# Kernel optimization log

Hardware: AMD Instinct MI355X
Metric: run time of the kernel (lower is better)

Reference implementation:

```python
import jax, jax.numpy as jnp
import numpy as np

N_HEAD = 16
D = 1024
LV = 2048
HEAD_DIM = D // N_HEAD
B = 2
LQ = 2048
LN_EPS = 1e-5


def setup_inputs() -> dict:
    key = jax.random.key(0)
    ks = jax.random.split(key, 8)
    s = 0.02
    v = jax.random.normal(ks[0], (B, LV, D), dtype=jnp.float32)
    q = jax.random.normal(ks[1], (B, LQ, D), dtype=jnp.float32)
    # per-head attn linear: d -> lv
    Wa = jax.random.normal(ks[2], (N_HEAD, D, LV), dtype=jnp.float32) * s
    ba = jnp.zeros((N_HEAD, LV), dtype=jnp.float32)
    # per-head layernorm over d
    gamma = jnp.ones((N_HEAD, D), dtype=jnp.float32)
    beta = jnp.zeros((N_HEAD, D), dtype=jnp.float32)
    # per-head proj (FilteredLinear modeled as affine): d -> head_dim
    Wp = jax.random.normal(ks[3], (N_HEAD, D, HEAD_DIM), dtype=jnp.float32) * s
    bp = jnp.zeros((N_HEAD, HEAD_DIM), dtype=jnp.float32)
    return {"v": v, "q": q, "Wa": Wa, "ba": ba, "gamma": gamma,
            "beta": beta, "Wp": Wp, "bp": bp}


def _mha(v, q, Wa, ba, gamma, beta, Wp, bp):
    # attn: [H, B, Lq, Lv] = relu(q @ Wa_h + ba_h)  (batched across heads)
    attn = jax.nn.relu(jnp.einsum('bqd,hdl->hbql', q, Wa)
                       + ba[:, None, None, :])
    # external-attention aggregation: [H, B, Lq, D]
    agg = jnp.einsum('hbql,bld->hbqd', attn, v)
    # per-head LayerNorm over last dim (d)
    mu = jnp.mean(agg, axis=-1, keepdims=True)
    var = jnp.var(agg, axis=-1, keepdims=True)
    normed = (agg - mu) * jax.lax.rsqrt(var + LN_EPS)
    normed = normed * gamma[:, None, None, :] + beta[:, None, None, :]
    # per-head projection to head_dim: [H, B, Lq, head_dim]
    heads = jnp.einsum('hbqd,hde->hbqe', normed, Wp) + bp[:, None, None, :]
    # concat heads along feature dim -> [B, Lq, D]
    return heads.transpose(1, 2, 0, 3).reshape(q.shape[0], q.shape[1], -1)


def reference(v, q, Wa, ba, gamma, beta, Wp, bp):
    return _mha(v, q, Wa, ba, gamma, beta, Wp, bp)
```

## Files before the change

kernel.cpp:

```cpp
#include <hip/hip_runtime.h>
#include <hip/hip_bf16.h>

typedef __attribute__((ext_vector_type(8))) short short8;
typedef __attribute__((ext_vector_type(4))) float f32x4;

#define N_HEAD 16
#define DMODEL 1024
#define LV 2048
#define LQ 2048
#define BATCH 2
#define HEAD_DIM 64

template <int N> struct IC { static constexpr int v = N; };

__device__ inline ushort f2bf(float f) {
    union { float f; unsigned u; } v; v.f = f;
    unsigned r = v.u + 0x7fffu + ((v.u >> 16) & 1u);
    return (ushort)(r >> 16);
}
__device__ inline float bf2f(ushort h) {
    union { unsigned u; float f; } v; v.u = ((unsigned)h) << 16;
    return v.f;
}

__global__ __launch_bounds__(256) void cast_bf16(const float* __restrict__ src,
                                                 ushort* __restrict__ dst, int n) {
    int i = (blockIdx.x * 256 + threadIdx.x) * 4;
    if (i < n) {
        float4 v = *(const float4*)(src + i);
        ushort4 o;
        o.x = f2bf(v.x); o.y = f2bf(v.y); o.z = f2bf(v.z); o.w = f2bf(v.w);
        *(ushort4*)(dst + i) = o;
    }
}

__global__ __launch_bounds__(256) void transpose_cast(const float* __restrict__ src,
                                                      ushort* __restrict__ dst,
                                                      int R, int C) {
    __shared__ float t[32][33];
    size_t zoff = (size_t)blockIdx.z * R * C;
    int c0 = blockIdx.x * 32, r0 = blockIdx.y * 32;
    int tx = threadIdx.x, ty = threadIdx.y;
#pragma unroll
    for (int i = 0; i < 4; ++i)
        t[ty + i * 8][tx] = src[zoff + (size_t)(r0 + ty + i * 8) * C + c0 + tx];
    __syncthreads();
#pragma unroll
    for (int i = 0; i < 4; ++i)
        dst[zoff + (size_t)(c0 + ty + i * 8) * R + r0 + tx] = f2bf(t[tx][ty + i * 8]);
}

template <bool RELU>
__global__ __launch_bounds__(512, 4) void gemm128x256(
    const ushort* __restrict__ A, const ushort* __restrict__ B,
    ushort* __restrict__ Cout, const float* __restrict__ bias,
    int K,
    long sA_b, long sA_h, long sB_b, long sB_h, long sC_z, int ldc, long sBias_h)
{
    __shared__ __align__(16) char smem[3 * 24576];

    const int z = blockIdx.z, b = z & 1, h = z >> 1;
    A += (size_t)b * sA_b + (size_t)h * sA_h;
    B += (size_t)b * sB_b + (size_t)h * sB_h;
    const float* biasp = bias ? bias + (size_t)h * sBias_h : nullptr;

    const int bm0 = blockIdx.y * 128;
    const int bn0 = blockIdx.x * 256;
    const int T = threadIdx.x;
    const int lane = T & 63, wid = T >> 6;
    const int wr = wid >> 2, wc = wid & 3;
    const int fr = lane & 15, fq = lane >> 4;
    const int laneoff = fr * 64 + ((fq * 16) ^ ((fr >> 3) << 5));

    const int s_row = T >> 2;
    const int s_csw = ((T & 3) * 16) ^ (((T >> 5) & 1) << 5);
    const ushort* gA = A + (size_t)(bm0 + s_row) * K + (s_csw >> 1);
    const ushort* gB = B + (size_t)(bn0 + s_row) * K + (s_csw >> 1);

    const int nt = K >> 5;

    auto stage = [&](int sb, int kt) {
        char* base = smem + sb * 24576;
        const ushort* srcA = gA + (size_t)kt * 32;
        __builtin_amdgcn_global_load_lds(
            (const __attribute__((address_space(1))) void*)srcA,
            (__attribute__((address_space(3))) void*)(base + (T << 4)), 16, 0, 0);
#pragma unroll
        for (int j = 0; j < 2; ++j) {
            const ushort* srcB = gB + (size_t)j * 128 * K + (size_t)kt * 32;
            __builtin_amdgcn_global_load_lds(
                (const __attribute__((address_space(1))) void*)srcB,
                (__attribute__((address_space(3))) void*)(base + 8192 + j * 8192 + (T << 4)),
                16, 0, 0);
        }
    };

    f32x4 acc[4][4];
#pragma unroll
    for (int m = 0; m < 4; ++m)
#pragma unroll
        for (int n = 0; n < 4; ++n)
#pragma unroll
            for (int j = 0; j < 4; ++j) acc[m][n][j] = 0.f;

    auto step = [&](int t, int rb, int sb, auto DOST, auto VM) {
        const char* base = smem + rb * 24576;
        const char* pA = base + wr * 4096 + laneoff;
        const char* pB = base + 8192 + wc * 4096 + laneoff;
        short8 a[4], bb[4];
#pragma unroll
        for (int m = 0; m < 4; ++m) a[m] = *(const short8*)(pA + m * 1024);
#pragma unroll
        for (int n = 0; n < 4; ++n) bb[n] = *(const short8*)(pB + n * 1024);
        if constexpr (decltype(DOST)::v) stage(sb, t + 2);
        asm volatile("s_waitcnt lgkmcnt(0)" ::: "memory");
        __builtin_amdgcn_sched_barrier(0);
        __builtin_amdgcn_s_setprio(1);
#pragma unroll
        for (int m = 0; m < 4; ++m)
#pragma unroll
            for (int n = 0; n < 4; ++n)
                acc[m][n] = __builtin_amdgcn_mfma_f32_16x16x32_bf16(
                    a[m], bb[n], acc[m][n], 0, 0, 0);
        __builtin_amdgcn_s_setprio(0);
        __builtin_amdgcn_sched_barrier(0);
        constexpr int vm = decltype(VM)::v;
        if constexpr (vm == 3) asm volatile("s_waitcnt vmcnt(3)" ::: "memory");
        else if constexpr (vm == 0) asm volatile("s_waitcnt vmcnt(0)" ::: "memory");
        if constexpr (vm >= 0) asm volatile("s_barrier" ::: "memory");
    };

    stage(0, 0); stage(1, 1);
    asm volatile("s_waitcnt vmcnt(3)" ::: "memory");
    asm volatile("s_barrier" ::: "memory");

    int rb = 0, sb = 2;
    for (int t = 0; t < nt - 2; ++t) {
        step(t, rb, sb, IC<1>{}, IC<3>{});
        rb = (rb == 2) ? 0 : rb + 1;
        sb = (sb == 2) ? 0 : sb + 1;
    }
    step(nt - 2, rb, sb, IC<0>{}, IC<0>{});
    rb = (rb == 2) ? 0 : rb + 1;
    step(nt - 1, rb, sb, IC<0>{}, IC<-1>{});

    ushort* C = Cout + (size_t)z * sC_z;
    const int row0 = bm0 + wr * 64;
    const int col0 = bn0 + wc * 64;
#pragma unroll
    for (int n = 0; n < 4; ++n) {
        const int c = col0 + n * 16 + fr;
        const float bvv = biasp ? biasp[c] : 0.f;
#pragma unroll
        for (int m = 0; m < 4; ++m) {
            const int r = row0 + m * 16 + fq * 4;
#pragma unroll
            for (int j = 0; j < 4; ++j) {
                float val = acc[m][n][j] + bvv;
                if (RELU) val = fmaxf(val, 0.f);
                C[(size_t)(r + j) * ldc + c] = f2bf(val);
            }
        }
    }
}

__global__ __launch_bounds__(256) void ln_kernel(ushort* __restrict__ agg,
                                                 const float* __restrict__ gamma,
                                                 const float* __restrict__ beta) {
    const int wid = threadIdx.x >> 6, lane = threadIdx.x & 63;
    const size_t row = (size_t)blockIdx.x * 4 + wid;
    const int h = (int)(row >> 12);
    ushort* p = agg + row * 1024 + lane * 16;
    short8 r0 = *(const short8*)p;
    short8 r1 = *(const short8*)(p + 8);
    float x[16];
#pragma unroll
    for (int j = 0; j < 8; ++j) { x[j] = bf2f((ushort)r0[j]); x[8 + j] = bf2f((ushort)r1[j]); }
    float s = 0.f, s2 = 0.f;
#pragma unroll
    for (int j = 0; j < 16; ++j) { s += x[j]; s2 += x[j] * x[j]; }
    for (int o = 1; o < 64; o <<= 1) {
        s  += __shfl_xor(s,  o, 64);
        s2 += __shfl_xor(s2, o, 64);
    }
    float mu  = s * (1.0f / 1024.0f);
    float var = s2 * (1.0f / 1024.0f) - mu * mu;
    float rs  = rsqrtf(fmaxf(var, 0.f) + 1e-5f);
    const float* g  = gamma + (size_t)h * 1024 + lane * 16;
    const float* bt = beta  + (size_t)h * 1024 + lane * 16;
    short8 o0, o1;
#pragma unroll
    for (int j = 0; j < 8; ++j) {
        o0[j] = (short)f2bf((x[j]     - mu) * rs * g[j]     + bt[j]);
        o1[j] = (short)f2bf((x[8 + j] - mu) * rs * g[8 + j] + bt[8 + j]);
    }
    *(short8*)p = o0;
    *(short8*)(p + 8) = o1;
}

__global__ __launch_bounds__(256) void proj_kernel(const ushort* __restrict__ normed,
                                                   const ushort* __restrict__ WpT,
                                                   const float* __restrict__ bp,
                                                   float* __restrict__ out,
                                                   int h_base) {
    const int z = blockIdx.y, b = z & 1, h = z >> 1;
    const int hg = h_base + h;
    const int wid = threadIdx.x >> 6, lane = threadIdx.x & 63;
    const int fr = lane & 15, fq = lane >> 4;
    const int m0 = (blockIdx.x * 4 + wid) * 16;

    const ushort* Abase = normed + ((size_t)z * 2048 + m0 + fr) * 1024 + fq * 8;
    const ushort* Bbase = WpT + (size_t)hg * 64 * 1024 + (size_t)fr * 1024 + fq * 8;

    f32x4 acc[4];
#pragma unroll
    for (int n = 0; n < 4; ++n)
#pragma unroll
        for (int j = 0; j < 4; ++j) acc[n][j] = 0.f;

    for (int kt = 0; kt < 32; ++kt) {
        short8 a = *(const short8*)(Abase + kt * 32);
#pragma unroll
        for (int n = 0; n < 4; ++n) {
            short8 bb = *(const short8*)(Bbase + n * 16 * 1024 + kt * 32);
            acc[n] = __builtin_amdgcn_mfma_f32_16x16x32_bf16(a, bb, acc[n], 0, 0, 0);
        }
    }
#pragma unroll
    for (int n = 0; n < 4; ++n) {
        int c = hg * 64 + n * 16 + fr;
        float bvv = bp[hg * 64 + n * 16 + fr];
#pragma unroll
        for (int j = 0; j < 4; ++j)
            out[(size_t)b * 2048 * 1024 + (size_t)(m0 + fq * 4 + j) * 1024 + c] =
                acc[n][j] + bvv;
    }
}

extern "C" void kernel_launch(void* const* d_in, const int* in_sizes, int n_in,
                              void* d_out, int out_size, void* d_ws, size_t ws_size,
                              hipStream_t stream) {
    const float* v     = (const float*)d_in[0];
    const float* q     = (const float*)d_in[1];
    const float* Wa    = (const float*)d_in[2];
    const float* ba    = (const float*)d_in[3];
    const float* gamma = (const float*)d_in[4];
    const float* beta  = (const float*)d_in[5];
    const float* Wp    = (const float*)d_in[6];
    const float* bp    = (const float*)d_in[7];
    float* out = (float*)d_out;

    const size_t MB = 1ull << 20;
    char* ws = (char*)d_ws;
    ushort* qbf = (ushort*)(ws);
    ushort* vT  = (ushort*)(ws + 8 * MB);
    ushort* WpT = (ushort*)(ws + 16 * MB);
    int NH = 1;
    {
        const int cands[5] = {16, 8, 4, 2, 1};
        for (int i = 0; i < 5; ++i) {
            if ((size_t)(18 + 28 * cands[i]) * MB <= ws_size) { NH = cands[i]; break; }
        }
    }
    ushort* WaT_c  = (ushort*)(ws + 18 * MB);
    ushort* attn_c = (ushort*)(ws + (18 + (size_t)4 * NH) * MB);
    ushort* agg_c  = (ushort*)(ws + (18 + (size_t)20 * NH) * MB);

    dim3 tb(32, 8);
    cast_bf16<<<4096, 256, 0, stream>>>(q, qbf, BATCH * LQ * DMODEL);
    transpose_cast<<<dim3(DMODEL / 32, LV / 32, BATCH), tb, 0, stream>>>(v, vT, LV, DMODEL);
    transpose_cast<<<dim3(HEAD_DIM / 32, DMODEL / 32, N_HEAD), tb, 0, stream>>>(Wp, WpT, DMODEL, HEAD_DIM);

    for (int h0 = 0; h0 < N_HEAD; h0 += NH) {
        transpose_cast<<<dim3(LV / 32, DMODEL / 32, NH), tb, 0, stream>>>(
            Wa + (size_t)h0 * DMODEL * LV, WaT_c, DMODEL, LV);

        gemm128x256<true><<<dim3(LV / 256, LQ / 128, NH * 2), 512, 0, stream>>>(
            qbf, WaT_c, attn_c, ba + (size_t)h0 * LV, DMODEL,
            (long)LQ * DMODEL, 0L,
            0L, (long)LV * DMODEL,
            (long)LQ * LV, LV, (long)LV);

        gemm128x256<false><<<dim3(DMODEL / 256, LQ / 128, NH * 2), 512, 0, stream>>>(
            attn_c, vT, agg_c, nullptr, LV,
            (long)LQ * LV, (long)2 * LQ * LV,
            (long)DMODEL * LV, 0L,
            (long)LQ * DMODEL, DMODEL, 0L);

        ln_kernel<<<(NH * 2 * LQ) / 4, 256, 0, stream>>>(
            agg_c, gamma + (size_t)h0 * DMODEL, beta + (size_t)h0 * DMODEL);

        proj_kernel<<<dim3(LQ / 64, NH * 2), 256, 0, stream>>>(
            agg_c, WpT, bp, out, h0);
    }
}
```

Before: 845.3 us.

## Fuse LayerNorm into projection, stage GEMM epilogue via LDS, remap block order for XCDs

```diff
diff --git a/kernel.cpp b/kernel.cpp
--- a/kernel.cpp
+++ b/kernel.cpp
@@ -50,7 +50,7 @@
         dst[zoff + (size_t)(c0 + ty + i * 8) * R + r0 + tx] = f2bf(t[tx][ty + i * 8]);
 }
 
-template <bool RELU>
+template <bool RELU, int LNBN, int ZSH>
 __global__ __launch_bounds__(512, 4) void gemm128x256(
     const ushort* __restrict__ A, const ushort* __restrict__ B,
     ushort* __restrict__ Cout, const float* __restrict__ bias,
@@ -59,13 +59,19 @@
 {
     __shared__ __align__(16) char smem[3 * 24576];
 
-    const int z = blockIdx.z, b = z & 1, h = z >> 1;
+    const int gid = blockIdx.x;
+    const int per = (int)gridDim.x >> 3;
+    const int w = (gid & 7) * per + (gid >> 3);
+    const int z = w >> ZSH;
+    const int rem = w & ((1 << ZSH) - 1);
+    const int bm0 = (rem >> LNBN) * 128;
+    const int bn0 = (rem & ((1 << LNBN) - 1)) * 256;
+
+    const int b = z & 1, h = z >> 1;
     A += (size_t)b * sA_b + (size_t)h * sA_h;
     B += (size_t)b * sB_b + (size_t)h * sB_h;
     const float* biasp = bias ? bias + (size_t)h * sBias_h : nullptr;
 
-    const int bm0 = blockIdx.y * 128;
-    const int bn0 = blockIdx.x * 256;
     const int T = threadIdx.x;
     const int lane = T & 63, wid = T >> 6;
     const int wr = wid >> 2, wc = wid & 3;
@@ -144,73 +150,63 @@
     rb = (rb == 2) ? 0 : rb + 1;
     step(nt - 1, rb, sb, IC<0>{}, IC<-1>{});
 
-    ushort* C = Cout + (size_t)z * sC_z;
+    asm volatile("s_waitcnt vmcnt(0) lgkmcnt(0)" ::: "memory");
+    __builtin_amdgcn_s_barrier();
+    char* eb = smem + wid * 9216;
     const int row0 = bm0 + wr * 64;
     const int col0 = bn0 + wc * 64;
 #pragma unroll
     for (int n = 0; n < 4; ++n) {
-        const int c = col0 + n * 16 + fr;
-        const float bvv = biasp ? biasp[c] : 0.f;
+        const float bvv = biasp ? biasp[col0 + n * 16 + fr] : 0.f;
 #pragma unroll
         for (int m = 0; m < 4; ++m) {
-            const int r = row0 + m * 16 + fq * 4;
 #pragma unroll
             for (int j = 0; j < 4; ++j) {
                 float val = acc[m][n][j] + bvv;
                 if (RELU) val = fmaxf(val, 0.f);
-                C[(size_t)(r + j) * ldc + c] = f2bf(val);
+                *(ushort*)(eb + (m * 16 + fq * 4 + j) * 144 + (n * 16 + fr) * 2) = f2bf(val);
             }
         }
     }
-}
-
-__global__ __launch_bounds__(256) void ln_kernel(ushort* __restrict__ agg,
-                                                 const float* __restrict__ gamma,
-                                                 const float* __restrict__ beta) {
-    const int wid = threadIdx.x >> 6, lane = threadIdx.x & 63;
-    const size_t row = (size_t)blockIdx.x * 4 + wid;
-    const int h = (int)(row >> 12);
-    ushort* p = agg + row * 1024 + lane * 16;
-    short8 r0 = *(const short8*)p;
-    short8 r1 = *(const short8*)(p + 8);
-    float x[16];
-#pragma unroll
-    for (int j = 0; j < 8; ++j) { x[j] = bf2f((ushort)r0[j]); x[8 + j] = bf2f((ushort)r1[j]); }
-    float s = 0.f, s2 = 0.f;
-#pragma unroll
-    for (int j = 0; j < 16; ++j) { s += x[j]; s2 += x[j] * x[j]; }
-    for (int o = 1; o < 64; o <<= 1) {
-        s  += __shfl_xor(s,  o, 64);
-        s2 += __shfl_xor(s2, o, 64);
-    }
-    float mu  = s * (1.0f / 1024.0f);
-    float var = s2 * (1.0f / 1024.0f) - mu * mu;
-    float rs  = rsqrtf(fmaxf(var, 0.f) + 1e-5f);
-    const float* g  = gamma + (size_t)h * 1024 + lane * 16;
-    const float* bt = beta  + (size_t)h * 1024 + lane * 16;
-    short8 o0, o1;
-#pragma unroll
-    for (int j = 0; j < 8; ++j) {
-        o0[j] = (short)f2bf((x[j]     - mu) * rs * g[j]     + bt[j]);
-        o1[j] = (short)f2bf((x[8 + j] - mu) * rs * g[8 + j] + bt[8 + j]);
-    }
-    *(short8*)p = o0;
-    *(short8*)(p + 8) = o1;
-}
-
-__global__ __launch_bounds__(256) void proj_kernel(const ushort* __restrict__ normed,
-                                                   const ushort* __restrict__ WpT,
-                                                   const float* __restrict__ bp,
-                                                   float* __restrict__ out,
-                                                   int h_base) {
-    const int z = blockIdx.y, b = z & 1, h = z >> 1;
-    const int hg = h_base + h;
+    asm volatile("s_waitcnt lgkmcnt(0)" ::: "memory");
+    ushort* C = Cout + (size_t)z * sC_z;
+    const int rl = lane >> 3, cb = lane & 7;
+#pragma unroll
+    for (int i = 0; i < 8; ++i) {
+        short8 vv = *(const short8*)(eb + (i * 8 + rl) * 144 + cb * 16);
+        *(short8*)(C + (size_t)(row0 + i * 8 + rl) * ldc + col0 + cb * 8) = vv;
+    }
+}
+
+__global__ __launch_bounds__(256) void lnproj_kernel(const ushort* __restrict__ agg,
+                                                     const ushort* __restrict__ WpT,
+                                                     const float* __restrict__ gamma,
+                                                     const float* __restrict__ beta,
+                                                     const float* __restrict__ bp,
+                                                     float* __restrict__ out,
+                                                     int h_base) {
+    const int z = blockIdx.y, b = z & 1, hg = h_base + (z >> 1);
     const int wid = threadIdx.x >> 6, lane = threadIdx.x & 63;
     const int fr = lane & 15, fq = lane >> 4;
     const int m0 = (blockIdx.x * 4 + wid) * 16;
 
-    const ushort* Abase = normed + ((size_t)z * 2048 + m0 + fr) * 1024 + fq * 8;
+    const ushort* Arow = agg + ((size_t)z * 2048 + m0 + fr) * 1024 + fq * 8;
+
+    float s = 0.f, s2 = 0.f;
+    for (int kt = 0; kt < 32; ++kt) {
+        short8 a = *(const short8*)(Arow + kt * 32);
+#pragma unroll
+        for (int j = 0; j < 8; ++j) { float x = bf2f((ushort)a[j]); s += x; s2 += x * x; }
+    }
+    s  += __shfl_xor(s, 16, 64);  s2 += __shfl_xor(s2, 16, 64);
+    s  += __shfl_xor(s, 32, 64);  s2 += __shfl_xor(s2, 32, 64);
+    const float mu  = s * (1.0f / 1024.0f);
+    const float var = s2 * (1.0f / 1024.0f) - mu * mu;
+    const float rs  = rsqrtf(fmaxf(var, 0.f) + 1e-5f);
+
     const ushort* Bbase = WpT + (size_t)hg * 64 * 1024 + (size_t)fr * 1024 + fq * 8;
+    const float* gp = gamma + (size_t)hg * 1024 + fq * 8;
+    const float* bt = beta  + (size_t)hg * 1024 + fq * 8;
 
     f32x4 acc[4];
 #pragma unroll
@@ -219,17 +215,29 @@
         for (int j = 0; j < 4; ++j) acc[n][j] = 0.f;
 
     for (int kt = 0; kt < 32; ++kt) {
-        short8 a = *(const short8*)(Abase + kt * 32);
+        short8 a = *(const short8*)(Arow + kt * 32);
+        float4 g0 = *(const float4*)(gp + kt * 32);
+        float4 g1 = *(const float4*)(gp + kt * 32 + 4);
+        float4 b0 = *(const float4*)(bt + kt * 32);
+        float4 b1 = *(const float4*)(bt + kt * 32 + 4);
+        const float gg[8] = {g0.x, g0.y, g0.z, g0.w, g1.x, g1.y, g1.z, g1.w};
+        const float bb_[8] = {b0.x, b0.y, b0.z, b0.w, b1.x, b1.y, b1.z, b1.w};
+        short8 an;
+#pragma unroll
+        for (int j = 0; j < 8; ++j) {
+            float xn = (bf2f((ushort)a[j]) - mu) * rs * gg[j] + bb_[j];
+            an[j] = (short)f2bf(xn);
+        }
 #pragma unroll
         for (int n = 0; n < 4; ++n) {
-            short8 bb = *(const short8*)(Bbase + n * 16 * 1024 + kt * 32);
-            acc[n] = __builtin_amdgcn_mfma_f32_16x16x32_bf16(a, bb, acc[n], 0, 0, 0);
+            short8 wv = *(const short8*)(Bbase + n * 16 * 1024 + kt * 32);
+            acc[n] = __builtin_amdgcn_mfma_f32_16x16x32_bf16(an, wv, acc[n], 0, 0, 0);
         }
     }
 #pragma unroll
     for (int n = 0; n < 4; ++n) {
-        int c = hg * 64 + n * 16 + fr;
-        float bvv = bp[hg * 64 + n * 16 + fr];
+        const int c = hg * 64 + n * 16 + fr;
+        const float bvv = bp[c];
 #pragma unroll
         for (int j = 0; j < 4; ++j)
             out[(size_t)b * 2048 * 1024 + (size_t)(m0 + fq * 4 + j) * 1024 + c] =
@@ -275,22 +283,19 @@
         transpose_cast<<<dim3(LV / 32, DMODEL / 32, NH), tb, 0, stream>>>(
             Wa + (size_t)h0 * DMODEL * LV, WaT_c, DMODEL, LV);
 
-        gemm128x256<true><<<dim3(LV / 256, LQ / 128, NH * 2), 512, 0, stream>>>(
+        gemm128x256<true, 3, 7><<<128 * NH * 2, 512, 0, stream>>>(
             qbf, WaT_c, attn_c, ba + (size_t)h0 * LV, DMODEL,
             (long)LQ * DMODEL, 0L,
             0L, (long)LV * DMODEL,
             (long)LQ * LV, LV, (long)LV);
 
-        gemm128x256<false><<<dim3(DMODEL / 256, LQ / 128, NH * 2), 512, 0, stream>>>(
+        gemm128x256<false, 2, 6><<<64 * NH * 2, 512, 0, stream>>>(
             attn_c, vT, agg_c, nullptr, LV,
             (long)LQ * LV, (long)2 * LQ * LV,
             (long)DMODEL * LV, 0L,
             (long)LQ * DMODEL, DMODEL, 0L);
 
-        ln_kernel<<<(NH * 2 * LQ) / 4, 256, 0, stream>>>(
-            agg_c, gamma + (size_t)h0 * DMODEL, beta + (size_t)h0 * DMODEL);
-
-        proj_kernel<<<dim3(LQ / 64, NH * 2), 256, 0, stream>>>(
-            agg_c, WpT, bp, out, h0);
-    }
-}
+        lnproj_kernel<<<dim3(LQ / 64, NH * 2), 256, 0, stream>>>(
+            agg_c, WpT, gamma, beta, bp, out, h0);
+    }
+}
```

Measured after the change: 754.6 us. 1.12x faster.
